# Optimization experiments

Measured on AMD Instinct MI355X. Metric: run time of the kernel, lower is better.

## Reference

```python
import jax, jax.numpy as jnp
import numpy as np

B, C, N = 8, 512, 2048

def setup_inputs() -> dict:
    key = jax.random.key(0)
    ks = jax.random.split(key, 7)
    s = 1.0 / np.sqrt(C)
    return {
        "x": jax.random.normal(ks[0], (B, C, N), dtype=jnp.float32),
        "wq": jax.random.normal(ks[1], (C, C), dtype=jnp.float32) * s,
        "bq": jax.random.normal(ks[2], (C,), dtype=jnp.float32) * s,
        "wk": jax.random.normal(ks[3], (C, C), dtype=jnp.float32) * s,
        "bk": jax.random.normal(ks[4], (C,), dtype=jnp.float32) * s,
        "wv": jax.random.normal(ks[5], (C, C), dtype=jnp.float32) * s,
        "bv": jax.random.normal(ks[6], (C,), dtype=jnp.float32) * s,
    }

def reference(x, wq, bq, wk, bk, wv, bv):
    # Conv1d with kernel=1 == pointwise channel matmul: [B,C,N] -> [B,C,N]
    q = jnp.einsum('oc,bcn->bon', wq, x) + bq[None, :, None]
    k = jnp.einsum('oc,bcn->bon', wk, x) + bk[None, :, None]
    v = jnp.einsum('oc,bcn->bon', wv, x) + bv[None, :, None]
    # scores[b,i,j] = sum_c q[b,c,i] * k[b,c,j]; softmax over j (no scaling, as in source)
    scores = jnp.einsum('bci,bcj->bij', q, k)
    attn = jax.nn.softmax(scores, axis=-1)  # [B,N,N]
    # out[b,c,i] = sum_j v[b,c,j] * attn[b,i,j]
    out = jnp.einsum('bcj,bij->bci', v, attn)
    return out + x
```

## Files before the change

kernel.cpp:

```cpp
#include <hip/hip_runtime.h>
#include <hip/hip_bf16.h>

typedef _Float16 half_t;
typedef _Float16 f16x8 __attribute__((ext_vector_type(8)));
typedef float f32x4 __attribute__((ext_vector_type(4)));

#define AS1 __attribute__((address_space(1)))
#define AS3 __attribute__((address_space(3)))

constexpr int CB = 512;
constexpr int NB = 2048;
constexpr int BB = 8;

__device__ inline f32x4 mfma16(f16x8 a, f16x8 b, f32x4 c) {
  return __builtin_amdgcn_mfma_f32_16x16x32_f16(a, b, c, 0, 0, 0);
}

__global__ void convert_w(const float* __restrict__ wv, half_t* __restrict__ wvh) {
  int i = blockIdx.x * 256 + threadIdx.x;
  if (i < CB * CB) wvh[i] = (half_t)wv[i];
}

__global__ __launch_bounds__(256) void compute_G_part(const float* __restrict__ wq,
                                                      const float* __restrict__ wk,
                                                      float* __restrict__ Gp) {
  __shared__ float aq[64][68];
  __shared__ float ak[64][68];
  const int c0 = blockIdx.y * 64, d0 = blockIdx.x * 64, o0 = blockIdx.z * 64;
  const int t = threadIdx.x;
  {
    const int r = t >> 2, cbase = (t & 3) * 16;
    const float* q = wq + (size_t)(o0 + r) * CB + c0 + cbase;
    const float* k = wk + (size_t)(o0 + r) * CB + d0 + cbase;
#pragma unroll
    for (int q4 = 0; q4 < 4; q4++) {
      *(float4*)&aq[r][cbase + q4 * 4] = *(const float4*)(q + q4 * 4);
      *(float4*)&ak[r][cbase + q4 * 4] = *(const float4*)(k + q4 * 4);
    }
  }
  __syncthreads();
  const int tc = t & 15, td = t >> 4;
  float acc[4][4] = {};
#pragma unroll 8
  for (int o = 0; o < 64; o++) {
    float4 a4 = *(const float4*)&aq[o][tc * 4];
    float4 b4 = *(const float4*)&ak[o][td * 4];
    float av[4] = {a4.x, a4.y, a4.z, a4.w};
    float bv[4] = {b4.x, b4.y, b4.z, b4.w};
#pragma unroll
    for (int i = 0; i < 4; i++)
#pragma unroll
      for (int j = 0; j < 4; j++)
        acc[i][j] += av[i] * bv[j];
  }
  float* gz = Gp + (size_t)blockIdx.z * CB * CB;
#pragma unroll
  for (int i = 0; i < 4; i++) {
    int c = c0 + tc * 4 + i;
#pragma unroll
    for (int j = 0; j < 4; j++)
      gz[(size_t)c * CB + d0 + td * 4 + j] = acc[i][j];
  }
}

__global__ void reduce_G(const float* __restrict__ Gp,
                         half_t* __restrict__ Gh, half_t* __restrict__ Gl) {
  int i = blockIdx.x * 256 + threadIdx.x;
  if (i >= CB * CB) return;
  float s = 0.0f;
#pragma unroll
  for (int z = 0; z < 8; z++) s += Gp[(size_t)z * CB * CB + i];
  half_t h = (half_t)s;
  Gh[i] = h;
  Gl[i] = (half_t)(s - (float)h);
}

__global__ void compute_u(const float* __restrict__ wk, const float* __restrict__ bq,
                          float* __restrict__ u) {
  int d = blockIdx.x * 256 + threadIdx.x;
  if (d >= CB) return;
  float s = 0.0f;
  for (int o = 0; o < CB; o++) s += bq[o] * wk[(size_t)o * CB + d];
  u[d] = s;
}

__global__ __launch_bounds__(256) void compute_ubias(const half_t* __restrict__ xh,
                                                     const float* __restrict__ u,
                                                     float* __restrict__ ub) {
  __shared__ float us[CB];
  for (int i = threadIdx.x; i < CB; i += 256) us[i] = u[i];
  __syncthreads();
  int row = blockIdx.x * 4 + (threadIdx.x >> 6);
  int lane = threadIdx.x & 63;
  f16x8 vh = *(const f16x8*)(xh + (size_t)row * CB + lane * 8);
  float s = 0.0f;
#pragma unroll
  for (int i = 0; i < 8; i++) s += us[lane * 8 + i] * (float)vh[i];
#pragma unroll
  for (int off = 32; off; off >>= 1) s += __shfl_xor(s, off);
  if (lane == 0) ub[row] = s;
}

__global__ void transpose_x(const float* __restrict__ x, half_t* __restrict__ oh) {
  __shared__ float tile[32][33];
  int b = blockIdx.z, c0 = blockIdx.y * 32, n0 = blockIdx.x * 32;
  int tx = threadIdx.x, ty = threadIdx.y;
  const float* xb = x + (size_t)b * CB * NB;
#pragma unroll
  for (int r = 0; r < 4; r++)
    tile[ty + 8 * r][tx] = xb[(size_t)(c0 + ty + 8 * r) * NB + n0 + tx];
  __syncthreads();
  size_t base = (size_t)b * NB * CB;
#pragma unroll
  for (int r = 0; r < 4; r++)
    oh[base + (size_t)(n0 + ty + 8 * r) * CB + c0 + tx] = (half_t)tile[tx][ty + 8 * r];
}

template <int BIAS, int EPI, int BSPLIT>
__global__ __launch_bounds__(256) void gemm_nt(
    const half_t* __restrict__ A, int lda, long sA,
    const half_t* __restrict__ Bh, const half_t* __restrict__ Bl, int ldb, long sB,
    void* __restrict__ D, int ldd, long sD,
    const float* __restrict__ bias, long sBias,
    const float* __restrict__ R, int ldr, long sR,
    int K) {
  constexpr int PL = 2 + BSPLIT;
  constexpr int TSZ = 128 * 32;
  __shared__ alignas(16) half_t sm[2 * PL * TSZ];

  const int t = threadIdx.x;
  const int z = blockIdx.z;
  const half_t* Ab  = A  + (size_t)z * sA + (size_t)(blockIdx.y * 128) * lda;
  const half_t* Bbh = Bh + (size_t)z * sB + (size_t)(blockIdx.x * 128) * ldb;
  const half_t* Bbl = BSPLIT ? Bl + (size_t)z * sB + (size_t)(blockIdx.x * 128) * ldb : nullptr;
  const int wid = t >> 6, l15 = t & 15, hi = (t >> 4) & 3;
  const int wr = wid >> 1, wc = wid & 1;
  const int lineA = t >> 2, eoff = (t & 3) * 8;

  f32x4 acc[4][4] = {};

  auto stage = [&](int buf, int kt) {
    half_t* base = sm + buf * (PL * TSZ);
#pragma unroll
    for (int p = 0; p < 2; p++) {
      size_t goA = (size_t)(p * 64 + lineA) * lda + kt * 32 + eoff;
      size_t goB = (size_t)(p * 64 + lineA) * ldb + kt * 32 + eoff;
      int lo = p * 2048 + t * 8;
      __builtin_amdgcn_global_load_lds((const AS1 void*)(Ab + goA),  (AS3 void*)(base + lo), 16, 0, 0);
      __builtin_amdgcn_global_load_lds((const AS1 void*)(Bbh + goB), (AS3 void*)(base + TSZ + lo), 16, 0, 0);
      if (BSPLIT)
        __builtin_amdgcn_global_load_lds((const AS1 void*)(Bbl + goB), (AS3 void*)(base + 2 * TSZ + lo), 16, 0, 0);
    }
  };

  const int nt = K >> 5;
  stage(0, 0);
  __syncthreads();
  int cur = 0;
  for (int kt = 0; kt < nt; kt++) {
    if (kt + 1 < nt) stage(cur ^ 1, kt + 1);
    const half_t* bb = sm + cur * (PL * TSZ);
    f16x8 af[4], bfh[4], bfl[4];
#pragma unroll
    for (int f = 0; f < 4; f++) {
      int ao = (wr * 64 + f * 16 + l15) * 32 + hi * 8;
      int bo = (wc * 64 + f * 16 + l15) * 32 + hi * 8;
      af[f]  = *(const f16x8*)(bb + ao);
      bfh[f] = *(const f16x8*)(bb + TSZ + bo);
      if (BSPLIT) bfl[f] = *(const f16x8*)(bb + 2 * TSZ + bo);
    }
#pragma unroll
    for (int pass = 0; pass < 1 + BSPLIT; pass++) {
#pragma unroll
      for (int fm = 0; fm < 4; fm++)
#pragma unroll
        for (int fn = 0; fn < 4; fn++)
          acc[fm][fn] = mfma16(af[fm], (pass == 1) ? bfl[fn] : bfh[fn], acc[fm][fn]);
    }
    __syncthreads();
    cur ^= 1;
  }

  const int row0 = blockIdx.y * 128 + wr * 64;
  const int col0 = blockIdx.x * 128 + wc * 64;
#pragma unroll
  for (int fm = 0; fm < 4; fm++) {
    int rowb = row0 + fm * 16 + hi * 4;
#pragma unroll
    for (int fn = 0; fn < 4; fn++) {
      int col = col0 + fn * 16 + l15;
      float bc = (BIAS == 1) ? bias[(size_t)z * sBias + col] : 0.0f;
#pragma unroll
      for (int r = 0; r < 4; r++) {
        float val = acc[fm][fn][r] + bc;
        if (BIAS == 2) val += bias[(size_t)z * sBias + rowb + r];
        size_t di = (size_t)(rowb + r) * ldd + col;
        if (EPI == 0) {
          ((float*)D)[(size_t)z * sD + di] = val;
        } else if (EPI == 1) {
          ((half_t*)D)[(size_t)z * sD + di] = (half_t)val;
        } else {
          val += R[(size_t)z * sR + (size_t)(rowb + r) * ldr + col];
          ((float*)D)[(size_t)z * sD + di] = val;
        }
      }
    }
  }
}

struct alignas(16) H8 { half_t h[8]; };

__global__ __launch_bounds__(256) void softmax_rows(float* __restrict__ S) {
  float* row = S + (size_t)blockIdx.x * NB;
  int t = threadIdx.x;
  float4 v0 = ((const float4*)row)[t * 2];
  float4 v1 = ((const float4*)row)[t * 2 + 1];
  float vals[8] = {v0.x, v0.y, v0.z, v0.w, v1.x, v1.y, v1.z, v1.w};
  float m = vals[0];
#pragma unroll
  for (int i = 1; i < 8; i++) m = fmaxf(m, vals[i]);
#pragma unroll
  for (int off = 32; off; off >>= 1) m = fmaxf(m, __shfl_xor(m, off));
  __shared__ float redm[4], reds[4];
  if ((t & 63) == 0) redm[t >> 6] = m;
  __syncthreads();
  m = fmaxf(fmaxf(redm[0], redm[1]), fmaxf(redm[2], redm[3]));
  float e[8], s = 0.0f;
#pragma unroll
  for (int i = 0; i < 8; i++) { e[i] = __expf(vals[i] - m); s += e[i]; }
#pragma unroll
  for (int off = 32; off; off >>= 1) s += __shfl_xor(s, off);
  if ((t & 63) == 0) reds[t >> 6] = s;
  __syncthreads();
  s = reds[0] + reds[1] + reds[2] + reds[3];
  float inv = 1.0f / s;
  H8 ob;
#pragma unroll
  for (int i = 0; i < 8; i++) ob.h[i] = (half_t)(e[i] * inv);
  *reinterpret_cast<H8*>(reinterpret_cast<char*>(row) + t * 16) = ob;
}

extern "C" void kernel_launch(void* const* d_in, const int* in_sizes, int n_in,
                              void* d_out, int out_size, void* d_ws, size_t ws_size,
                              hipStream_t stream) {
  const float* x  = (const float*)d_in[0];
  const float* wq = (const float*)d_in[1];
  const float* bq = (const float*)d_in[2];
  const float* wk = (const float*)d_in[3];
  const float* wv = (const float*)d_in[5];
  const float* bv = (const float*)d_in[6];
  float* out = (float*)d_out;

  const size_t MB = 1u << 20;
  if (ws_size < 180 * MB) return;

  char* ws = (char*)d_ws;
  half_t* xh   = (half_t*)(ws + 0);
  half_t* YTh  = (half_t*)(ws + 16 * MB);
  half_t* v    = (half_t*)(ws + 32 * MB);
  float*  S    = (float*)(ws + 48 * MB);
  float*  Gp   = (float*)(ws + 48 * MB);
  half_t* Gh   = (half_t*)(ws + 176 * MB);
  half_t* Gl   = (half_t*)(ws + 176 * MB + 512 * 1024);
  half_t* wvh  = (half_t*)(ws + 177 * MB);
  float*  u    = (float*)(ws + 177 * MB + 512 * 1024);
  float*  ub   = (float*)(ws + 177 * MB + 768 * 1024);

  convert_w<<<1024, 256, 0, stream>>>(wv, wvh);
  compute_G_part<<<dim3(8, 8, 8), 256, 0, stream>>>(wq, wk, Gp);
  reduce_G<<<1024, 256, 0, stream>>>(Gp, Gh, Gl);
  compute_u<<<2, 256, 0, stream>>>(wk, bq, u);
  transpose_x<<<dim3(64, 16, 8), dim3(32, 8), 0, stream>>>(x, xh);
  compute_ubias<<<BB * NB / 4, 256, 0, stream>>>(xh, u, ub);

  gemm_nt<0, 1, 1><<<dim3(4, 16, 8), 256, 0, stream>>>(
      xh, CB, (long)NB * CB, Gh, Gl, CB, 0,
      YTh, CB, (long)NB * CB, nullptr, 0, nullptr, 0, 0, CB);

  gemm_nt<2, 1, 0><<<dim3(16, 4, 8), 256, 0, stream>>>(
      wvh, CB, 0, xh, nullptr, CB, (long)NB * CB,
      v, NB, (long)CB * NB, bv, 0, nullptr, 0, 0, CB);

  gemm_nt<1, 0, 0><<<dim3(16, 16, 8), 256, 0, stream>>>(
      xh, CB, (long)NB * CB,
      YTh, nullptr, CB, (long)NB * CB,
      S, NB, (long)NB * NB, ub, NB, nullptr, 0, 0, CB);

  softmax_rows<<<BB * NB, 256, 0, stream>>>(S);

  gemm_nt<0, 2, 0><<<dim3(16, 4, 8), 256, 0, stream>>>(
      v, NB, (long)CB * NB,
      (const half_t*)S, nullptr, 2 * NB, (long)NB * 2 * NB,
      out, NB, (long)CB * NB, nullptr, 0,
      x, NB, (long)CB * NB, NB);
}
```

Measured before the change: 227.2 us.

## Add wide 128x256 GEMM tile, drop Gl split, write softmax to separate buffer

Adds a new gemm_wide kernel with a 128x256 block tile, double-buffered LDS via global_load_lds, and 4x8 MFMA fragments per wave. It replaces the score GEMM and the attention-times-V GEMM. The hi/lo fp16 split of G is removed, so the Y GEMM uses only the single half matrix, halving its MFMA work at some cost in precision. Softmax now writes fp16 probabilities to a separate contiguous buffer rather than in place, which gives the final GEMM a dense stride. The larger tile raises register pressure (128 accumulator floats per thread) and may lower occupancy.

New measurement: 258.7 us. 1.14x slower.

```diff
diff --git a/kernel.cpp b/kernel.cpp
--- a/kernel.cpp
+++ b/kernel.cpp
@@ -63,16 +63,13 @@
   }
 }
 
-__global__ void reduce_G(const float* __restrict__ Gp,
-                         half_t* __restrict__ Gh, half_t* __restrict__ Gl) {
+__global__ void reduce_G(const float* __restrict__ Gp, half_t* __restrict__ Gh) {
   int i = blockIdx.x * 256 + threadIdx.x;
   if (i >= CB * CB) return;
   float s = 0.0f;
 #pragma unroll
   for (int z = 0; z < 8; z++) s += Gp[(size_t)z * CB * CB + i];
-  half_t h = (half_t)s;
-  Gh[i] = h;
-  Gl[i] = (half_t)(s - (float)h);
+  Gh[i] = (half_t)s;
 }
 
 __global__ void compute_u(const float* __restrict__ wk, const float* __restrict__ bq,
@@ -208,10 +205,93 @@
   }
 }
 
+template <int BIAS, int EPI>
+__global__ __launch_bounds__(256) void gemm_wide(
+    const half_t* __restrict__ A, int lda, long sA,
+    const half_t* __restrict__ B, int ldb, long sB,
+    float* __restrict__ D, int ldd, long sD,
+    const float* __restrict__ bias, long sBias,
+    const float* __restrict__ R, int ldr, long sR,
+    int K) {
+  constexpr int ATSZ = 128 * 32;
+  constexpr int BTSZ = 256 * 32;
+  constexpr int BUF = ATSZ + BTSZ;
+  __shared__ alignas(16) half_t sm[2 * BUF];
+
+  const int t = threadIdx.x;
+  const int z = blockIdx.z;
+  const half_t* Ab = A + (size_t)z * sA + (size_t)(blockIdx.y * 128) * lda;
+  const half_t* Bb = B + (size_t)z * sB + (size_t)(blockIdx.x * 256) * ldb;
+  const int wid = t >> 6, l15 = t & 15, hi = (t >> 4) & 3;
+  const int wr = wid >> 1, wc = wid & 1;
+  const int lineA = t >> 2, eoff = (t & 3) * 8;
+
+  f32x4 acc[4][8] = {};
+
+  auto stage = [&](int buf, int kt) {
+    half_t* base = sm + buf * BUF;
+#pragma unroll
+    for (int p = 0; p < 2; p++) {
+      size_t goA = (size_t)(p * 64 + lineA) * lda + kt * 32 + eoff;
+      __builtin_amdgcn_global_load_lds((const AS1 void*)(Ab + goA),
+                                       (AS3 void*)(base + p * 2048 + t * 8), 16, 0, 0);
+    }
+#pragma unroll
+    for (int p = 0; p < 4; p++) {
+      size_t goB = (size_t)(p * 64 + lineA) * ldb + kt * 32 + eoff;
+      __builtin_amdgcn_global_load_lds((const AS1 void*)(Bb + goB),
+                                       (AS3 void*)(base + ATSZ + p * 2048 + t * 8), 16, 0, 0);
+    }
+  };
+
+  const int nt = K >> 5;
+  stage(0, 0);
+  __syncthreads();
+  int cur = 0;
+  for (int kt = 0; kt < nt; kt++) {
+    if (kt + 1 < nt) stage(cur ^ 1, kt + 1);
+    const half_t* bb = sm + cur * BUF;
+    f16x8 af[4], bf[8];
+#pragma unroll
+    for (int f = 0; f < 4; f++)
+      af[f] = *(const f16x8*)(bb + (wr * 64 + f * 16 + l15) * 32 + hi * 8);
+#pragma unroll
+    for (int f = 0; f < 8; f++)
+      bf[f] = *(const f16x8*)(bb + ATSZ + (wc * 128 + f * 16 + l15) * 32 + hi * 8);
+#pragma unroll
+    for (int fm = 0; fm < 4; fm++)
+#pragma unroll
+      for (int fn = 0; fn < 8; fn++)
+        acc[fm][fn] = mfma16(af[fm], bf[fn], acc[fm][fn]);
+    __syncthreads();
+    cur ^= 1;
+  }
+
+  const int row0 = blockIdx.y * 128 + wr * 64;
+  const int col0 = blockIdx.x * 256 + wc * 128;
+#pragma unroll
+  for (int fm = 0; fm < 4; fm++) {
+    int rowb = row0 + fm * 16 + hi * 4;
+#pragma unroll
+    for (int fn = 0; fn < 8; fn++) {
+      int col = col0 + fn * 16 + l15;
+      float bc = (BIAS == 1) ? bias[(size_t)z * sBias + col] : 0.0f;
+#pragma unroll
+      for (int r = 0; r < 4; r++) {
+        float val = acc[fm][fn][r] + bc;
+        size_t di = (size_t)(rowb + r) * ldd + col;
+        if (EPI == 2) val += R[(size_t)z * sR + (size_t)(rowb + r) * ldr + col];
+        D[(size_t)z * sD + di] = val;
+      }
+    }
+  }
+}
+
 struct alignas(16) H8 { half_t h[8]; };
 
-__global__ __launch_bounds__(256) void softmax_rows(float* __restrict__ S) {
-  float* row = S + (size_t)blockIdx.x * NB;
+__global__ __launch_bounds__(256) void softmax_rows(const float* __restrict__ S,
+                                                    half_t* __restrict__ P) {
+  const float* row = S + (size_t)blockIdx.x * NB;
   int t = threadIdx.x;
   float4 v0 = ((const float4*)row)[t * 2];
   float4 v1 = ((const float4*)row)[t * 2 + 1];
@@ -237,7 +317,7 @@
   H8 ob;
 #pragma unroll
   for (int i = 0; i < 8; i++) ob.h[i] = (half_t)(e[i] * inv);
-  *reinterpret_cast<H8*>(reinterpret_cast<char*>(row) + t * 16) = ob;
+  *reinterpret_cast<H8*>(P + (size_t)blockIdx.x * NB + t * 8) = ob;
 }
 
 extern "C" void kernel_launch(void* const* d_in, const int* in_sizes, int n_in,
@@ -252,7 +332,7 @@
   float* out = (float*)d_out;
 
   const size_t MB = 1u << 20;
-  if (ws_size < 180 * MB) return;
+  if (ws_size < 243 * MB) return;
 
   char* ws = (char*)d_ws;
   half_t* xh   = (half_t*)(ws + 0);
@@ -260,37 +340,35 @@
   half_t* v    = (half_t*)(ws + 32 * MB);
   float*  S    = (float*)(ws + 48 * MB);
   float*  Gp   = (float*)(ws + 48 * MB);
-  half_t* Gh   = (half_t*)(ws + 176 * MB);
-  half_t* Gl   = (half_t*)(ws + 176 * MB + 512 * 1024);
-  half_t* wvh  = (half_t*)(ws + 177 * MB);
-  float*  u    = (float*)(ws + 177 * MB + 512 * 1024);
-  float*  ub   = (float*)(ws + 177 * MB + 768 * 1024);
+  half_t* Pd   = (half_t*)(ws + 176 * MB);
+  half_t* Gh   = (half_t*)(ws + 240 * MB);
+  half_t* wvh  = (half_t*)(ws + 240 * MB + 512 * 1024);
+  float*  u    = (float*)(ws + 241 * MB);
+  float*  ub   = (float*)(ws + 241 * MB + 256 * 1024);
 
   convert_w<<<1024, 256, 0, stream>>>(wv, wvh);
   compute_G_part<<<dim3(8, 8, 8), 256, 0, stream>>>(wq, wk, Gp);
-  reduce_G<<<1024, 256, 0, stream>>>(Gp, Gh, Gl);
+  reduce_G<<<1024, 256, 0, stream>>>(Gp, Gh);
   compute_u<<<2, 256, 0, stream>>>(wk, bq, u);
   transpose_x<<<dim3(64, 16, 8), dim3(32, 8), 0, stream>>>(x, xh);
   compute_ubias<<<BB * NB / 4, 256, 0, stream>>>(xh, u, ub);
 
-  gemm_nt<0, 1, 1><<<dim3(4, 16, 8), 256, 0, stream>>>(
-      xh, CB, (long)NB * CB, Gh, Gl, CB, 0,
+  gemm_nt<0, 1, 0><<<dim3(4, 16, 8), 256, 0, stream>>>(
+      xh, CB, (long)NB * CB, Gh, nullptr, CB, 0,
       YTh, CB, (long)NB * CB, nullptr, 0, nullptr, 0, 0, CB);
 
   gemm_nt<2, 1, 0><<<dim3(16, 4, 8), 256, 0, stream>>>(
       wvh, CB, 0, xh, nullptr, CB, (long)NB * CB,
       v, NB, (long)CB * NB, bv, 0, nullptr, 0, 0, CB);
 
-  gemm_nt<1, 0, 0><<<dim3(16, 16, 8), 256, 0, stream>>>(
-      xh, CB, (long)NB * CB,
-      YTh, nullptr, CB, (long)NB * CB,
+  gemm_wide<1, 0><<<dim3(8, 16, 8), 256, 0, stream>>>(
+      xh, CB, (long)NB * CB, YTh, CB, (long)NB * CB,
       S, NB, (long)NB * NB, ub, NB, nullptr, 0, 0, CB);
 
-  softmax_rows<<<BB * NB, 256, 0, stream>>>(S);
-
-  gemm_nt<0, 2, 0><<<dim3(16, 4, 8), 256, 0, stream>>>(
-      v, NB, (long)CB * NB,
-      (const half_t*)S, nullptr, 2 * NB, (long)NB * 2 * NB,
+  softmax_rows<<<BB * NB, 256, 0, stream>>>(S, Pd);
+
+  gemm_wide<0, 2><<<dim3(8, 4, 8), 256, 0, stream>>>(
+      v, NB, (long)CB * NB, Pd, NB, (long)NB * NB,
       out, NB, (long)CB * NB, nullptr, 0,
       x, NB, (long)CB * NB, NB);
 }
```

## Store attention scores as fixed-point int16 and drop the split-precision G GEMM

Applied to the files above, without the earlier changes.

The score GEMM now writes its logits as 16-bit fixed point (scaled by 256 and clamped) instead of fp32. Softmax reads these shorts and writes fp16 probabilities to a separate dense buffer, so the score traffic through memory is halved and the PV GEMM reads a contiguous layout. The G matrix is now stored only as a single fp16 value, which removes the hi/lo compensation pass from the projection GEMM. The cost is accuracy: scores are quantized to steps of 1/256 and clamp at about ±128, and G loses its extra precision.

After: 207.4 us. 8.7% less time.

```diff
diff --git a/kernel.cpp b/kernel.cpp
--- a/kernel.cpp
+++ b/kernel.cpp
@@ -63,16 +63,13 @@
   }
 }
 
-__global__ void reduce_G(const float* __restrict__ Gp,
-                         half_t* __restrict__ Gh, half_t* __restrict__ Gl) {
+__global__ void reduce_G(const float* __restrict__ Gp, half_t* __restrict__ Gh) {
   int i = blockIdx.x * 256 + threadIdx.x;
   if (i >= CB * CB) return;
   float s = 0.0f;
 #pragma unroll
   for (int z = 0; z < 8; z++) s += Gp[(size_t)z * CB * CB + i];
-  half_t h = (half_t)s;
-  Gh[i] = h;
-  Gl[i] = (half_t)(s - (float)h);
+  Gh[i] = (half_t)s;
 }
 
 __global__ void compute_u(const float* __restrict__ wk, const float* __restrict__ bq,
@@ -199,9 +196,12 @@
           ((float*)D)[(size_t)z * sD + di] = val;
         } else if (EPI == 1) {
           ((half_t*)D)[(size_t)z * sD + di] = (half_t)val;
-        } else {
+        } else if (EPI == 2) {
           val += R[(size_t)z * sR + (size_t)(rowb + r) * ldr + col];
           ((float*)D)[(size_t)z * sD + di] = val;
+        } else {
+          float sv = fminf(fmaxf(val * 256.0f, -32767.0f), 32767.0f);
+          ((short*)D)[(size_t)z * sD + di] = (short)__float2int_rn(sv);
         }
       }
     }
@@ -209,13 +209,16 @@
 }
 
 struct alignas(16) H8 { half_t h[8]; };
-
-__global__ __launch_bounds__(256) void softmax_rows(float* __restrict__ S) {
-  float* row = S + (size_t)blockIdx.x * NB;
+struct alignas(16) S8 { short s[8]; };
+
+__global__ __launch_bounds__(256) void softmax_rows(const short* __restrict__ S,
+                                                    half_t* __restrict__ P) {
+  const short* row = S + (size_t)blockIdx.x * NB;
   int t = threadIdx.x;
-  float4 v0 = ((const float4*)row)[t * 2];
-  float4 v1 = ((const float4*)row)[t * 2 + 1];
-  float vals[8] = {v0.x, v0.y, v0.z, v0.w, v1.x, v1.y, v1.z, v1.w};
+  S8 r8 = *reinterpret_cast<const S8*>(row + t * 8);
+  float vals[8];
+#pragma unroll
+  for (int i = 0; i < 8; i++) vals[i] = (float)r8.s[i] * 0.00390625f;
   float m = vals[0];
 #pragma unroll
   for (int i = 1; i < 8; i++) m = fmaxf(m, vals[i]);
@@ -237,7 +240,7 @@
   H8 ob;
 #pragma unroll
   for (int i = 0; i < 8; i++) ob.h[i] = (half_t)(e[i] * inv);
-  *reinterpret_cast<H8*>(reinterpret_cast<char*>(row) + t * 16) = ob;
+  *reinterpret_cast<H8*>(P + (size_t)blockIdx.x * NB + t * 8) = ob;
 }
 
 extern "C" void kernel_launch(void* const* d_in, const int* in_sizes, int n_in,
@@ -258,39 +261,39 @@
   half_t* xh   = (half_t*)(ws + 0);
   half_t* YTh  = (half_t*)(ws + 16 * MB);
   half_t* v    = (half_t*)(ws + 32 * MB);
-  float*  S    = (float*)(ws + 48 * MB);
+  short*  Ss   = (short*)(ws + 48 * MB);
   float*  Gp   = (float*)(ws + 48 * MB);
+  half_t* Pd   = (half_t*)(ws + 112 * MB);
   half_t* Gh   = (half_t*)(ws + 176 * MB);
-  half_t* Gl   = (half_t*)(ws + 176 * MB + 512 * 1024);
-  half_t* wvh  = (half_t*)(ws + 177 * MB);
-  float*  u    = (float*)(ws + 177 * MB + 512 * 1024);
-  float*  ub   = (float*)(ws + 177 * MB + 768 * 1024);
+  half_t* wvh  = (half_t*)(ws + 176 * MB + 512 * 1024);
+  float*  u    = (float*)(ws + 177 * MB);
+  float*  ub   = (float*)(ws + 177 * MB + 256 * 1024);
 
   convert_w<<<1024, 256, 0, stream>>>(wv, wvh);
   compute_G_part<<<dim3(8, 8, 8), 256, 0, stream>>>(wq, wk, Gp);
-  reduce_G<<<1024, 256, 0, stream>>>(Gp, Gh, Gl);
+  reduce_G<<<1024, 256, 0, stream>>>(Gp, Gh);
   compute_u<<<2, 256, 0, stream>>>(wk, bq, u);
   transpose_x<<<dim3(64, 16, 8), dim3(32, 8), 0, stream>>>(x, xh);
   compute_ubias<<<BB * NB / 4, 256, 0, stream>>>(xh, u, ub);
 
-  gemm_nt<0, 1, 1><<<dim3(4, 16, 8), 256, 0, stream>>>(
-      xh, CB, (long)NB * CB, Gh, Gl, CB, 0,
+  gemm_nt<0, 1, 0><<<dim3(4, 16, 8), 256, 0, stream>>>(
+      xh, CB, (long)NB * CB, Gh, nullptr, CB, 0,
       YTh, CB, (long)NB * CB, nullptr, 0, nullptr, 0, 0, CB);
 
   gemm_nt<2, 1, 0><<<dim3(16, 4, 8), 256, 0, stream>>>(
       wvh, CB, 0, xh, nullptr, CB, (long)NB * CB,
       v, NB, (long)CB * NB, bv, 0, nullptr, 0, 0, CB);
 
-  gemm_nt<1, 0, 0><<<dim3(16, 16, 8), 256, 0, stream>>>(
+  gemm_nt<1, 4, 0><<<dim3(16, 16, 8), 256, 0, stream>>>(
       xh, CB, (long)NB * CB,
       YTh, nullptr, CB, (long)NB * CB,
-      S, NB, (long)NB * NB, ub, NB, nullptr, 0, 0, CB);
-
-  softmax_rows<<<BB * NB, 256, 0, stream>>>(S);
+      Ss, NB, (long)NB * NB, ub, NB, nullptr, 0, 0, CB);
+
+  softmax_rows<<<BB * NB, 256, 0, stream>>>(Ss, Pd);
 
   gemm_nt<0, 2, 0><<<dim3(16, 4, 8), 256, 0, stream>>>(
       v, NB, (long)CB * NB,
-      (const half_t*)S, nullptr, 2 * NB, (long)NB * 2 * NB,
+      Pd, nullptr, NB, (long)NB * NB,
       out, NB, (long)CB * NB, nullptr, 0,
       x, NB, (long)CB * NB, NB);
 }
```
